# Performance work log

Measured on AMD Instinct MI355X. Metric: run time of the kernel, lower is better.

The kernel has to match this reference:

```python
import jax, jax.numpy as jnp
import numpy as np

EMBED = 1024
HEADS = 16
HDIM = EMBED // HEADS
QLEN = 512
KLEN = 1024
BATCH = 8


def setup_inputs() -> dict:
    key = jax.random.key(0)
    ks = jax.random.split(key, 20)
    s = 0.02
    return {
        "query": jax.random.normal(ks[0], (QLEN, BATCH, EMBED), jnp.float32),
        "key": jax.random.normal(ks[1], (KLEN, BATCH, EMBED), jnp.float32),
        "value": jax.random.normal(ks[2], (KLEN, BATCH, EMBED), jnp.float32),
        "pos_embedding": jax.random.normal(ks[3], (KLEN, 1, EMBED), jnp.float32),
        "U": jax.random.normal(ks[4], (HEADS, HDIM), jnp.float32) * s,
        "V": jax.random.normal(ks[5], (HEADS, HDIM), jnp.float32) * s,
        "mask": jax.random.randint(ks[6], (QLEN, KLEN, 1), 0, 2) == 1,
        "padding_mask": jax.random.randint(ks[7], (BATCH, QLEN), 0, 2).astype(jnp.float32),
        "Wq": jax.random.normal(ks[8], (EMBED, EMBED), jnp.float32) * s,
        "bq": jnp.zeros((EMBED,), jnp.float32),
        "Wk": jax.random.normal(ks[9], (EMBED, EMBED), jnp.float32) * s,
        "bk": jnp.zeros((EMBED,), jnp.float32),
        "Wv": jax.random.normal(ks[10], (EMBED, EMBED), jnp.float32) * s,
        "bv": jnp.zeros((EMBED,), jnp.float32),
        "Wpos": jax.random.normal(ks[11], (EMBED, EMBED), jnp.float32) * s,
        "Wo": jax.random.normal(ks[12], (EMBED, EMBED), jnp.float32) * s,
        "bo": jnp.zeros((EMBED,), jnp.float32),
    }


def _rel_shift(x):
    # x: (q, k, b, h) -> Transformer-XL relative shift (pad/reshape trick)
    q, k, b, h = x.shape
    zero_pad = jnp.zeros((q, 1, b, h), x.dtype)
    x_padded = jnp.concatenate([zero_pad, x], axis=1)  # (q, k+1, b, h)
    x_padded = x_padded.reshape(k + 1, q, b, h)
    return x_padded[1:].reshape(q, k, b, h)


def _padding_mask(pad, q_len, k_len):
    # pad: (b, q) in {0,1}; returns bool (b, q, k) where True = masked
    pm = jnp.einsum('bq,bk->bqk', pad, pad)  # (b, q, q)
    if k_len > q_len:
        mem = jnp.ones((pad.shape[0], q_len, k_len - q_len), pad.dtype)
        pm = jnp.concatenate([mem, pm], axis=2)
    return pm == 0


def reference(query, key, value, pos_embedding, U, V, mask, padding_mask,
              Wq, bq, Wk, bk, Wv, bv, Wpos, Wo, bo):
    q_len, b, e = query.shape
    k_len = key.shape[0]
    d = jnp.asarray(np.sqrt(e), query.dtype)

    q = (query @ Wq + bq).reshape(q_len, b, HEADS, HDIM)
    k = (key @ Wk + bk).reshape(k_len, b, HEADS, HDIM)
    v = (value @ Wv + bv).reshape(k_len, b, HEADS, HDIM)
    R = (pos_embedding @ Wpos).reshape(-1, HEADS, HDIM)  # (k_len, h, d)

    content = jnp.einsum('qbhd,kbhd->qkbh', q + U, k)
    position = _rel_shift(jnp.einsum('qbhd,khd->qkbh', q + V, R))
    score = (content + position) / d  # (q, k, b, h)

    NEG = jnp.asarray(-1e20, score.dtype)
    score = jnp.where(mask[:, :, :, None], NEG, score)  # mask (q,k,1)->(q,k,1,1)
    pmask = _padding_mask(padding_mask, q_len, k_len)  # (b,q,k)
    pmask = jnp.transpose(pmask, (1, 2, 0))[:, :, :, None]  # (q,k,b,1)
    score = jnp.where(pmask, NEG, score)

    attn = jax.nn.softmax(score, axis=1)
    alpha = jnp.einsum('qkbh,kbhd->qbhd', attn, v).reshape(q_len, b, e)
    return alpha @ Wo + bo
```

## Files before the change

### kernel.cpp

```cpp
#include <hip/hip_runtime.h>

#define QLEN 512
#define KLEN 1024
#define BATCH 8
#define HEADS 16
#define HDIM 64
#define EMBED 1024

typedef __attribute__((ext_vector_type(4))) float f32x4;
typedef __attribute__((ext_vector_type(8))) short short8;
typedef unsigned short ushort_t;
typedef unsigned char uchar_t;
typedef unsigned int uint_t;

#define MFMA16(a, b, c) __builtin_amdgcn_mfma_f32_16x16x32_bf16((a), (b), (c), 0, 0, 0)

__device__ __forceinline__ float b2f(ushort_t u) {
    union { uint_t i; float f; } c; c.i = ((uint_t)u) << 16; return c.f;
}
__device__ __forceinline__ ushort_t f2b(float x) {
    union { float f; uint_t i; } c; c.f = x;
    return (ushort_t)((c.i + 0x8000u) >> 16);
}
__device__ __forceinline__ uint_t pk2(float lo, float hi) {
    return (uint_t)f2b(lo) | ((uint_t)f2b(hi) << 16);
}
__device__ __forceinline__ float ldf(const void* p, int idx, int f32m) {
    if (f32m) return ((const float*)p)[idx];
    return b2f(((const ushort_t*)p)[idx]);
}

typedef const __attribute__((address_space(1))) void async_src_t;
typedef __attribute__((address_space(3))) void async_dst_t;

__global__ __launch_bounds__(256) void detect_kernel(const void* mask, const void* pad, int* flags) {
    __shared__ int cnt[4];
    int tid = threadIdx.x;
    if (tid < 4) cnt[tid] = 0;
    __syncthreads();
    const uchar_t* mb = (const uchar_t*)mask;
    const uchar_t* pb = (const uchar_t*)pad;
    int lnz1 = 0, l3f1 = 0, l3f3 = 0, lpnz = 0;
    for (int off = tid; off < 4096; off += 256) {
        uchar_t v = mb[off];
        int m4 = off & 3;
        if (m4 != 0 && v != 0) lnz1++;
        if (m4 == 1 && v == 0x3F) l3f1++;
        if (m4 == 3 && v == 0x3F) l3f3++;
        uchar_t p = pb[off];
        if (m4 == 0 && p != 0) lpnz++;
    }
    atomicAdd(&cnt[0], lnz1); atomicAdd(&cnt[1], l3f1);
    atomicAdd(&cnt[2], l3f3); atomicAdd(&cnt[3], lpnz);
    __syncthreads();
    if (tid == 0) {
        flags[0] = (cnt[3] == 0) ? 1 : 0;
        int mm;
        if (cnt[0] == 0) mm = 0;
        else if (cnt[1] > 16) mm = 2;
        else if (cnt[2] > 16) mm = 3;
        else mm = 1;
        flags[1] = mm;
    }
}

__device__ __forceinline__ void conv_body(const void* __restrict__ src, ushort_t* __restrict__ dst,
                                          int i, int n8, int f32m) {
    if (i >= n8) return;
    if (f32m) {
        const float4* s = (const float4*)src + (size_t)i * 2;
        float4 a = s[0], b = s[1];
        uint4 o;
        o.x = pk2(a.x, a.y); o.y = pk2(a.z, a.w);
        o.z = pk2(b.x, b.y); o.w = pk2(b.z, b.w);
        ((uint4*)dst)[i] = o;
    } else {
        ((uint4*)dst)[i] = ((const uint4*)src)[i];
    }
}

__global__ __launch_bounds__(256) void prep_kernel(
    const void* q_in, ushort_t* qbf, const void* k_in, ushort_t* kbf,
    const void* v_in, ushort_t* vbf,
    const void* W0, const void* W1, const void* W2, const void* W3, const void* W4,
    ushort_t* T0, ushort_t* T1, ushort_t* T2, ushort_t* T3, ushort_t* T4,
    const int* flags) {
    __shared__ float tl[32][33];
    const int bid = blockIdx.x;
    const int tid = threadIdx.x;
    const int f32m = flags[0];
    if (bid < 2048) {
        conv_body(q_in, qbf, bid * 256 + tid, 524288, f32m);
    } else if (bid < 6144) {
        conv_body(k_in, kbf, (bid - 2048) * 256 + tid, 1048576, f32m);
    } else if (bid < 10240) {
        conv_body(v_in, vbf, (bid - 6144) * 256 + tid, 1048576, f32m);
    } else {
        int l = bid - 10240;
        int z = l >> 10, r = l & 1023;
        int bx = r & 31, by = r >> 5;
        const void* W; ushort_t* T;
        switch (z) {
            case 0: W = W0; T = T0; break;
            case 1: W = W1; T = T1; break;
            case 2: W = W2; T = T2; break;
            case 3: W = W3; T = T3; break;
            default: W = W4; T = T4; break;
        }
        int tx = tid & 31, ty = tid >> 5;
        int x = bx * 32 + tx;
        #pragma unroll
        for (int j = 0; j < 4; ++j) {
            int row = by * 32 + ty + j * 8;
            tl[ty + j * 8][tx] = ldf(W, row * 1024 + x, f32m);
        }
        __syncthreads();
        #pragma unroll
        for (int j = 0; j < 4; ++j) {
            int n = bx * 32 + ty + j * 8;
            T[n * 1024 + by * 32 + tx] = f2b(tl[tx][ty + j * 8]);
        }
    }
}

template<int EPI>
__device__ __forceinline__ void gemm_body(
    int mt, int nt, const void* Av, const ushort_t* BT,
    const void* bias, const void* Up, const void* Vp,
    void* out0, void* out1, const int* flags, int a_mode,
    ushort_t* As, ushort_t* Bs) {
    const int f32m = flags[0];
    const int a_f32 = a_mode ? f32m : 0;
    const int tid = threadIdx.x;
    const int wid = tid >> 6, lane = tid & 63;
    const int wr = (wid >> 1) * 64, wc = (wid & 1) * 64;
    const int m0 = mt * 128, n0 = nt * 128;
    const int ch0 = wid * 2;
    const int lrow = lane >> 2, lcol = (lane & 3) * 8;

    f32x4 acc[4][4];
    #pragma unroll
    for (int m = 0; m < 4; ++m)
        #pragma unroll
        for (int n = 0; n < 4; ++n)
            acc[m][n] = (f32x4){0.f, 0.f, 0.f, 0.f};

    for (int k0 = 0; k0 < 1024; k0 += 32) {
        if (a_f32) {
            const float* Af = (const float*)Av + (size_t)(m0 + (tid >> 1)) * 1024 + k0 + (tid & 1) * 16;
            ushort_t* dst = &As[(tid >> 1) * 32 + (tid & 1) * 16];
            #pragma unroll
            for (int e = 0; e < 16; ++e) dst[e] = f2b(Af[e]);
        } else {
            #pragma unroll
            for (int t = 0; t < 2; ++t) {
                int ch = ch0 + t;
                const ushort_t* ga = (const ushort_t*)Av + (size_t)(m0 + ch * 16 + lrow) * 1024 + k0 + lcol;
                __builtin_amdgcn_global_load_lds((async_src_t*)ga, (async_dst_t*)&As[ch * 512], 16, 0, 0);
            }
        }
        #pragma unroll
        for (int t = 0; t < 2; ++t) {
            int ch = ch0 + t;
            const ushort_t* gb = BT + (size_t)(n0 + ch * 16 + lrow) * 1024 + k0 + lcol;
            __builtin_amdgcn_global_load_lds((async_src_t*)gb, (async_dst_t*)&Bs[ch * 512], 16, 0, 0);
        }
        __syncthreads();

        short8 af[4], bf[4];
        #pragma unroll
        for (int m = 0; m < 4; ++m)
            af[m] = *(const short8*)&As[(wr + m * 16 + (lane & 15)) * 32 + (lane >> 4) * 8];
        #pragma unroll
        for (int n = 0; n < 4; ++n)
            bf[n] = *(const short8*)&Bs[(wc + n * 16 + (lane & 15)) * 32 + (lane >> 4) * 8];
        #pragma unroll
        for (int m = 0; m < 4; ++m)
            #pragma unroll
            for (int n = 0; n < 4; ++n)
                acc[m][n] = MFMA16(af[m], bf[n], acc[m][n]);
        __syncthreads();
    }

    #pragma unroll
    for (int n = 0; n < 4; ++n) {
        int gn = n0 + wc + n * 16 + (lane & 15);
        float bv_ = (EPI == 2) ? 0.f : ldf(bias, gn, f32m);
        float uu = 0.f, vv = 0.f;
        if (EPI == 0) { uu = ldf(Up, gn, f32m); vv = ldf(Vp, gn, f32m); }
        #pragma unroll
        for (int m = 0; m < 4; ++m) {
            #pragma unroll
            for (int j = 0; j < 4; ++j) {
                int gm = m0 + wr + m * 16 + (lane >> 4) * 4 + j;
                float c = acc[m][n][j] + bv_;
                if (EPI == 0) {
                    int q = gm >> 3, b = gm & 7;
                    int h = gn >> 6, d = gn & 63;
                    int bhk = b * 16 + h;
                    size_t addr = ((size_t)bhk * 32 + (q >> 4)) * 1024 + (size_t)(d >> 5) * 512
                                  + ((q & 15) * 4 + ((d >> 3) & 3)) * 8 + (d & 7);
                    ((ushort_t*)out0)[addr] = f2b((c + uu) * 0.03125f);
                    ((ushort_t*)out1)[addr] = f2b((c + vv) * 0.03125f);
                } else if (EPI == 1) {
                    int kk = gm >> 3, b = gm & 7;
                    int h = gn >> 6, d = gn & 63;
                    ((ushort_t*)out0)[((b * 16 + h) * 1024 + kk) * 64 + d] = f2b(c);
                } else if (EPI == 2) {
                    int h = gn >> 6, d = gn & 63;
                    int jr = gm;
                    size_t addr = (((((size_t)h * 8 + (jr >> 7)) * 8 + ((jr >> 4) & 7)) * 2 + (d >> 5)) * 64
                                   + ((jr & 15) * 4 + ((d >> 3) & 3))) * 8 + (d & 7);
                    ((ushort_t*)out0)[addr] = f2b(c);
                } else if (EPI == 4) {
                    int kk = gm >> 3, b = gm & 7;
                    int h = gn >> 6, d = gn & 63;
                    size_t addr = ((((((size_t)(b * 16 + h)) * 8 + (kk >> 7)) * 8 + ((kk >> 4) & 7)) * 2 + (d >> 5)) * 64
                                   + ((kk & 15) * 4 + ((d >> 3) & 3))) * 8 + (d & 7);
                    ((ushort_t*)out0)[addr] = f2b(c);
                } else {
                    if (f32m) ((float*)out0)[gm * 1024 + gn] = c;
                    else ((ushort_t*)out0)[gm * 1024 + gn] = f2b(c);
                }
            }
        }
    }
}

template<int EPI>
__global__ __launch_bounds__(256) void gemm_kernel(
    const void* Av, const ushort_t* BT, int M,
    const void* bias, const void* Up, const void* Vp,
    void* out0, void* out1, const int* flags, int a_mode) {
    __shared__ ushort_t As[4096];
    __shared__ ushort_t Bs[4096];
    gemm_body<EPI>(blockIdx.x, blockIdx.y, Av, BT, bias, Up, Vp, out0, out1, flags, a_mode, As, Bs);
}

__global__ __launch_bounds__(256) void proj1_kernel(
    const ushort_t* qbf, const ushort_t* WqT, const void* bq, const void* Up, const void* Vp,
    ushort_t* qUw, ushort_t* qVw,
    const ushort_t* kbf, const ushort_t* WkT, const void* bk, ushort_t* khw,
    const void* pos_raw, const ushort_t* WposT, ushort_t* Rlw,
    const int* flags) {
    __shared__ ushort_t As[4096];
    __shared__ ushort_t Bs[4096];
    const int bid = blockIdx.x;
    if (bid < 256) {
        gemm_body<0>(bid & 31, bid >> 5, qbf, WqT, bq, Up, Vp, qUw, qVw, flags, 0, As, Bs);
    } else if (bid < 768) {
        int l = bid - 256;
        gemm_body<4>(l & 63, l >> 6, kbf, WkT, bk, nullptr, nullptr, khw, nullptr, flags, 0, As, Bs);
    } else {
        int l = bid - 768;
        gemm_body<2>(l & 7, l >> 3, pos_raw, WposT, nullptr, nullptr, nullptr, Rlw, nullptr, flags, 1, As, Bs);
    }
}

__global__ __launch_bounds__(256) void preattn_kernel(
    const ushort_t* __restrict__ vh, ushort_t* __restrict__ vT,
    const void* __restrict__ mask, const void* __restrict__ pad,
    uint_t* __restrict__ bits, const int* flags) {
    __shared__ ushort_t t[64][68];
    const int bid = blockIdx.x;
    const int tid = threadIdx.x;
    if (bid < 2048) {
        int bh = bid >> 4;
        int k0 = (bid & 15) * 64;
        int r = tid >> 2, c0 = (tid & 3) * 16;
        const short8* src = (const short8*)&vh[((size_t)bh * 1024 + k0 + r) * 64 + c0];
        *(short8*)&t[r][c0] = src[0];
        *(short8*)&t[r][c0 + 8] = src[1];
        __syncthreads();
        ushort_t tmp[16];
        #pragma unroll
        for (int j = 0; j < 16; ++j) tmp[j] = t[c0 + j][r];
        int dm = r >> 4, cc = r & 15;
        #pragma unroll
        for (int tt = 0; tt < 2; ++tt) {
            int og = ((k0 + c0) >> 3) + tt;
            int kc = og >> 4, ch = (og >> 2) & 3, g = og & 3;
            size_t addr = ((((((size_t)bh * 8 + kc) * 4 + ch) * 4 + dm) * 64) + cc * 4 + g) * 8;
            *(short8*)&vT[addr] = *(short8*)&tmp[tt * 8];
        }
    } else {
        int tid2 = (bid - 2048) * 256 + tid;
        int w = tid2 & 31, q = (tid2 >> 5) & 511, b = tid2 >> 14;
        int mm = flags[1], f32m = flags[0];
        float padq = ldf(pad, b * 512 + q, f32m);
        uint_t word = 0;
        for (int j = 0; j < 32; ++j) {
            int k = w * 32 + j;
            size_t mi = (size_t)q * 1024 + k;
            int dead;
            if (mm == 1) dead = (((const uchar_t*)mask)[mi] != 0);
            else if (mm == 2) dead = (((const ushort_t*)mask)[mi] != 0);
            else dead = (((const uint_t*)mask)[mi] != 0);
            if (k >= 512) {
                float padk = ldf(pad, b * 512 + k - 512, f32m);
                if (padq == 0.f || padk == 0.f) dead = 1;
            }
            word |= ((uint_t)dead) << j;
        }
        bits[((b * 8 + (w >> 2)) * 512 + q) * 4 + (w & 3)] = word;
    }
}

#define SP_STR 1032
#define PB_STR 136
__global__ __launch_bounds__(512, 4) void attn_kernel(
    const ushort_t* __restrict__ qU, const ushort_t* __restrict__ qV,
    const ushort_t* __restrict__ khn, const ushort_t* __restrict__ vtn,
    const ushort_t* __restrict__ Rln, const uint_t* __restrict__ mbits,
    ushort_t* __restrict__ alpha) {

    __shared__ __align__(16) uchar_t uni[35104];
    ushort_t* sPos = (ushort_t*)uni;
    ushort_t* sPb  = (ushort_t*)uni;
    float*    sO   = (float*)uni;
    __shared__ float sred[2][8][16];
    __shared__ float ssinv[16];

    const int tid = threadIdx.x;
    const int wid = tid >> 6, lane = tid & 63;
    const int g = lane >> 4, c = lane & 15;
    const int qt = blockIdx.x;
    const int q0 = qt * 16;
    const int bh = blockIdx.y;
    const int b = bh >> 4, h = bh & 15;
    const int kbase = wid * 128;
    const int lch = (c * 4 + g) * 8;

    {
        size_t qvb = ((size_t)bh * 32 + qt) * 1024;
        short8 bva0 = *(const short8*)&qV[qvb + lch];
        short8 bva1 = *(const short8*)&qV[qvb + 512 + lch];
        int qtb = (qt == 31) ? 31 : qt + 1;
        int cb = (qt == 31) ? 15 : c;
        size_t qvb2 = ((size_t)bh * 32 + qtb) * 1024;
        short8 bvb0 = *(const short8*)&qV[qvb2 + (cb * 4 + g) * 8];
        short8 bvb1 = *(const short8*)&qV[qvb2 + 512 + (cb * 4 + g) * 8];
        #pragma unroll
        for (int m = 0; m < 8; ++m) {
            size_t rb = ((((size_t)h * 8 + wid) * 8 + m) * 2) * 512;
            short8 ra0 = *(const short8*)&Rln[rb + lch];
            short8 ra1 = *(const short8*)&Rln[rb + 512 + lch];
            f32x4 p0 = (f32x4){0.f, 0.f, 0.f, 0.f};
            p0 = MFMA16(ra0, bva0, p0);
            p0 = MFMA16(ra1, bva1, p0);
            f32x4 p1 = (f32x4){0.f, 0.f, 0.f, 0.f};
            p1 = MFMA16(ra0, bvb0, p1);
            p1 = MFMA16(ra1, bvb1, p1);
            uint2 w;
            w.x = pk2(p0[0], p0[1]);
            w.y = pk2(p0[2], p0[3]);
            *(uint2*)&sPos[c * SP_STR + kbase + m * 16 + g * 4] = w;
            if (c == 0) {
                uint2 x;
                x.x = pk2(p1[0], p1[1]);
                x.y = pk2(p1[2], p1[3]);
                *(uint2*)&sPos[16 * SP_STR + kbase + m * 16 + g * 4] = x;
            }
        }
    }

    f32x4 acc[8];
    {
        size_t qub = ((size_t)bh * 32 + qt) * 1024;
        short8 bu0 = *(const short8*)&qU[qub + lch];
        short8 bu1 = *(const short8*)&qU[qub + 512 + lch];
        #pragma unroll
        for (int m = 0; m < 8; ++m) {
            size_t kb = ((((size_t)bh * 8 + wid) * 8 + m) * 2) * 512;
            short8 ka0 = *(const short8*)&khn[kb + lch];
            short8 ka1 = *(const short8*)&khn[kb + 512 + lch];
            f32x4 t = (f32x4){0.f, 0.f, 0.f, 0.f};
            t = MFMA16(ka0, bu0, t);
            t = MFMA16(ka1, bu1, t);
            acc[m] = t;
        }
    }
    __syncthreads();

    const int q = q0 + c;
    uint4 mw = *(const uint4*)(mbits + ((size_t)(b * 8 + wid) * 512 + q) * 4);
    uint_t mwa[4] = {mw.x, mw.y, mw.z, mw.w};

    const int mbase = kbase - q0;
    float mx = -3.0e38f;
    #pragma unroll
    for (int m = 0; m < 8; ++m) {
        const int mb = mbase + m * 16;
        uint_t word = mwa[m >> 1];
        if (mb + 15 <= 512) {
            int a0 = c * SP_STR + mb + g * 4 - c + 511;
            #pragma unroll
            for (int jj = 0; jj < 4; ++jj) {
                float s = acc[m][jj] + b2f(sPos[a0 + jj]);
                if ((word >> ((m & 1) * 16 + g * 4 + jj)) & 1u) s = -1e20f;
                acc[m][jj] = s;
                mx = fmaxf(mx, s);
            }
        } else if (mb - 15 >= 514) {
            int a0 = (c + 1) * SP_STR + mb + g * 4 - c - 514;
            #pragma unroll
            for (int jj = 0; jj < 4; ++jj) {
                float s = acc[m][jj] + b2f(sPos[a0 + jj]);
                if ((word >> ((m & 1) * 16 + g * 4 + jj)) & 1u) s = -1e20f;
                acc[m][jj] = s;
                mx = fmaxf(mx, s);
            }
        } else {
            #pragma unroll
            for (int jj = 0; jj < 4; ++jj) {
                int delta = mb + g * 4 + jj - c;
                int wrap = (delta > 512) ? 1 : 0;
                int j = wrap ? (delta - 514) : (delta + 511);
                float pos = b2f(sPos[(c + wrap) * SP_STR + j]);
                if (delta == 513) pos = 0.f;
                float s = acc[m][jj] + pos;
                if ((word >> ((m & 1) * 16 + g * 4 + jj)) & 1u) s = -1e20f;
                acc[m][jj] = s;
                mx = fmaxf(mx, s);
            }
        }
    }
    mx = fmaxf(mx, __shfl_xor(mx, 16, 64));
    mx = fmaxf(mx, __shfl_xor(mx, 32, 64));
    if (lane < 16) sred[0][wid][c] = mx;
    __syncthreads();
    {
        float a0 = fmaxf(fmaxf(sred[0][0][c], sred[0][1][c]), fmaxf(sred[0][2][c], sred[0][3][c]));
        float a1 = fmaxf(fmaxf(sred[0][4][c], sred[0][5][c]), fmaxf(sred[0][6][c], sred[0][7][c]));
        mx = fmaxf(a0, a1);
    }

    float ls = 0.f;
    #pragma unroll
    for (int m = 0; m < 8; ++m) {
        float p0 = __expf(acc[m][0] - mx);
        float p1 = __expf(acc[m][1] - mx);
        float p2 = __expf(acc[m][2] - mx);
        float p3 = __expf(acc[m][3] - mx);
        ls += (p0 + p1) + (p2 + p3);
        uint2 w;
        w.x = pk2(p0, p1);
        w.y = pk2(p2, p3);
        *(uint2*)&sPb[(wid * 16 + c) * PB_STR + m * 16 + g * 4] = w;
    }
    ls += __shfl_xor(ls, 16, 64);
    ls += __shfl_xor(ls, 32, 64);
    if (lane < 16) sred[1][wid][c] = ls;

    short8 va[4][4];
    #pragma unroll
    for (int ch = 0; ch < 4; ++ch)
        #pragma unroll
        for (int dm = 0; dm < 4; ++dm)
            va[ch][dm] = *(const short8*)&vtn[((((((size_t)bh * 8 + wid) * 4 + ch) * 4 + dm) * 64) * 8) + lch];
    __syncthreads();
    float ls2;
    {
        float a0 = (sred[1][0][c] + sred[1][1][c]) + (sred[1][2][c] + sred[1][3][c]);
        float a1 = (sred[1][4][c] + sred[1][5][c]) + (sred[1][6][c] + sred[1][7][c]);
        ls2 = a0 + a1;
    }
    if (wid == 0 && lane < 16) ssinv[c] = 1.0f / ls2;

    f32x4 oacc[4];
    #pragma unroll
    for (int dm = 0; dm < 4; ++dm) oacc[dm] = (f32x4){0.f, 0.f, 0.f, 0.f};
    short8 pbv[4];
    #pragma unroll
    for (int ch = 0; ch < 4; ++ch)
        pbv[ch] = *(const short8*)&sPb[(wid * 16 + c) * PB_STR + ch * 32 + g * 8];
    #pragma unroll
    for (int ch = 0; ch < 4; ++ch)
        #pragma unroll
        for (int dm = 0; dm < 4; ++dm)
            oacc[dm] = MFMA16(va[ch][dm], pbv[ch], oacc[dm]);

    __syncthreads();
    #pragma unroll
    for (int dm = 0; dm < 4; ++dm)
        #pragma unroll
        for (int jj = 0; jj < 4; ++jj)
            sO[wid * 1088 + (dm * 16 + g * 4 + jj) * 17 + c] = oacc[dm][jj];
    __syncthreads();
    for (int e = tid; e < 1024; e += 512) {
        int d = e & 63, qq = e >> 6;
        float v = ((sO[d * 17 + qq] + sO[1088 + d * 17 + qq]) +
                   (sO[2176 + d * 17 + qq] + sO[3264 + d * 17 + qq])) +
                  ((sO[4352 + d * 17 + qq] + sO[5440 + d * 17 + qq]) +
                   (sO[6528 + d * 17 + qq] + sO[7616 + d * 17 + qq]));
        v *= ssinv[qq];
        alpha[((size_t)(q0 + qq) * 8 + b) * 1024 + h * 64 + d] = f2b(v);
    }
}

extern "C" void kernel_launch(void* const* d_in, const int* in_sizes, int n_in,
                              void* d_out, int out_size, void* d_ws, size_t ws_size,
                              hipStream_t stream) {
    char* ws = (char*)d_ws;
    int* flags = (int*)ws;
    ushort_t* WqT   = (ushort_t*)(ws + 1024);
    ushort_t* WkT   = WqT + 1048576;
    ushort_t* WvT   = WkT + 1048576;
    ushort_t* WposT = WvT + 1048576;
    ushort_t* WoT   = WposT + 1048576;
    ushort_t* qUw   = WoT + 1048576;
    ushort_t* qVw   = qUw + 4194304;
    ushort_t* khw   = qVw + 4194304;
    ushort_t* Rlw   = khw + 8388608;
    ushort_t* R1    = Rlw + 1048576;
    ushort_t* R2    = R1 + 4194304;
    ushort_t* R3    = R2 + 8388608;
    ushort_t* qbf = R1;
    ushort_t* alw = R1;
    ushort_t* kbf = R2;
    ushort_t* vhw = R2;
    ushort_t* vbf = R3;
    ushort_t* vTw = R3;
    uint_t* mbits = (uint_t*)WqT;

    detect_kernel<<<1, 256, 0, stream>>>(d_in[6], d_in[7], flags);
    prep_kernel<<<15360, 256, 0, stream>>>(
        d_in[0], qbf, d_in[1], kbf, d_in[2], vbf,
        d_in[8], d_in[10], d_in[12], d_in[14], d_in[15],
        WqT, WkT, WvT, WposT, WoT, flags);
    proj1_kernel<<<832, 256, 0, stream>>>(
        qbf, WqT, d_in[9], d_in[4], d_in[5], qUw, qVw,
        kbf, WkT, d_in[11], khw,
        d_in[3], WposT, Rlw, flags);
    gemm_kernel<1><<<dim3(64, 8), 256, 0, stream>>>(vbf, WvT, 8192, d_in[13], nullptr, nullptr, vhw, nullptr, flags, 0);
    preattn_kernel<<<2560, 256, 0, stream>>>(vhw, vTw, d_in[6], d_in[7], mbits, flags);
    attn_kernel<<<dim3(32, 128), 512, 0, stream>>>(qUw, qVw, khw, vTw, Rlw, mbits, alw);
    gemm_kernel<3><<<dim3(32, 8), 256, 0, stream>>>(alw, WoT, 4096, d_in[16], nullptr, nullptr, d_out, nullptr, flags, 0);
}
```

Baseline: 316.6 us.

## Fuse V projection with transpose and mask build; use 64-row tiles for small GEMMs

The V projection GEMM now writes directly into the transposed tiled layout that attention consumes, which removes the separate transpose pass and its extra global round trip. It is merged with the mask-bit construction into one launch. A 64x128-tile GEMM variant is added for the Q projection and the output projection, doubling their block counts so more compute units are busy on these M=4096 GEMMs. The cost is scattered epilogue stores for V and a lower per-block reuse in the smaller tiles.

```diff
diff --git a/kernel.cpp b/kernel.cpp
--- a/kernel.cpp
+++ b/kernel.cpp
@@ -126,8 +126,7 @@
 template<int EPI>
 __device__ __forceinline__ void gemm_body(
     int mt, int nt, const void* Av, const ushort_t* BT,
-    const void* bias, const void* Up, const void* Vp,
-    void* out0, void* out1, const int* flags, int a_mode,
+    const void* bias, void* out0, const int* flags, int a_mode,
     ushort_t* As, ushort_t* Bs) {
     const int f32m = flags[0];
     const int a_f32 = a_mode ? f32m : 0;
@@ -186,27 +185,13 @@
     for (int n = 0; n < 4; ++n) {
         int gn = n0 + wc + n * 16 + (lane & 15);
         float bv_ = (EPI == 2) ? 0.f : ldf(bias, gn, f32m);
-        float uu = 0.f, vv = 0.f;
-        if (EPI == 0) { uu = ldf(Up, gn, f32m); vv = ldf(Vp, gn, f32m); }
         #pragma unroll
         for (int m = 0; m < 4; ++m) {
             #pragma unroll
             for (int j = 0; j < 4; ++j) {
                 int gm = m0 + wr + m * 16 + (lane >> 4) * 4 + j;
                 float c = acc[m][n][j] + bv_;
-                if (EPI == 0) {
-                    int q = gm >> 3, b = gm & 7;
-                    int h = gn >> 6, d = gn & 63;
-                    int bhk = b * 16 + h;
-                    size_t addr = ((size_t)bhk * 32 + (q >> 4)) * 1024 + (size_t)(d >> 5) * 512
-                                  + ((q & 15) * 4 + ((d >> 3) & 3)) * 8 + (d & 7);
-                    ((ushort_t*)out0)[addr] = f2b((c + uu) * 0.03125f);
-                    ((ushort_t*)out1)[addr] = f2b((c + vv) * 0.03125f);
-                } else if (EPI == 1) {
-                    int kk = gm >> 3, b = gm & 7;
-                    int h = gn >> 6, d = gn & 63;
-                    ((ushort_t*)out0)[((b * 16 + h) * 1024 + kk) * 64 + d] = f2b(c);
-                } else if (EPI == 2) {
+                if (EPI == 2) {
                     int h = gn >> 6, d = gn & 63;
                     int jr = gm;
                     size_t addr = (((((size_t)h * 8 + (jr >> 7)) * 8 + ((jr >> 4) & 7)) * 2 + (d >> 5)) * 64
@@ -219,22 +204,95 @@
                                    + ((kk & 15) * 4 + ((d >> 3) & 3))) * 8 + (d & 7);
                     ((ushort_t*)out0)[addr] = f2b(c);
                 } else {
+                    int kk = gm >> 3, b = gm & 7;
+                    int h = gn >> 6, d = gn & 63;
+                    int bh = b * 16 + h;
+                    int kc = kk >> 7, ch2 = (kk >> 5) & 3, gg = (kk >> 3) & 3, e = kk & 7;
+                    int dm = d >> 4, cc = d & 15;
+                    size_t addr = ((((((size_t)bh * 8 + kc) * 4 + ch2) * 4 + dm) * 64) + cc * 4 + gg) * 8 + e;
+                    ((ushort_t*)out0)[addr] = f2b(c);
+                }
+            }
+        }
+    }
+}
+
+template<int EPI>
+__device__ __forceinline__ void gemm_body64(
+    int mt, int nt, const void* Av, const ushort_t* BT,
+    const void* bias, const void* Up, const void* Vp,
+    void* out0, void* out1, const int* flags,
+    ushort_t* As, ushort_t* Bs) {
+    const int f32m = flags[0];
+    const int tid = threadIdx.x;
+    const int wid = tid >> 6, lane = tid & 63;
+    const int wr = (wid >> 1) * 32, wc = (wid & 1) * 64;
+    const int m0 = mt * 64, n0 = nt * 128;
+    const int ch0 = wid * 2;
+    const int lrow = lane >> 2, lcol = (lane & 3) * 8;
+
+    f32x4 acc[2][4];
+    #pragma unroll
+    for (int m = 0; m < 2; ++m)
+        #pragma unroll
+        for (int n = 0; n < 4; ++n)
+            acc[m][n] = (f32x4){0.f, 0.f, 0.f, 0.f};
+
+    for (int k0 = 0; k0 < 1024; k0 += 32) {
+        {
+            const ushort_t* ga = (const ushort_t*)Av + (size_t)(m0 + wid * 16 + lrow) * 1024 + k0 + lcol;
+            __builtin_amdgcn_global_load_lds((async_src_t*)ga, (async_dst_t*)&As[wid * 512], 16, 0, 0);
+        }
+        #pragma unroll
+        for (int t = 0; t < 2; ++t) {
+            int ch = ch0 + t;
+            const ushort_t* gb = BT + (size_t)(n0 + ch * 16 + lrow) * 1024 + k0 + lcol;
+            __builtin_amdgcn_global_load_lds((async_src_t*)gb, (async_dst_t*)&Bs[ch * 512], 16, 0, 0);
+        }
+        __syncthreads();
+
+        short8 af[2], bf[4];
+        #pragma unroll
+        for (int m = 0; m < 2; ++m)
+            af[m] = *(const short8*)&As[(wr + m * 16 + (lane & 15)) * 32 + (lane >> 4) * 8];
+        #pragma unroll
+        for (int n = 0; n < 4; ++n)
+            bf[n] = *(const short8*)&Bs[(wc + n * 16 + (lane & 15)) * 32 + (lane >> 4) * 8];
+        #pragma unroll
+        for (int m = 0; m < 2; ++m)
+            #pragma unroll
+            for (int n = 0; n < 4; ++n)
+                acc[m][n] = MFMA16(af[m], bf[n], acc[m][n]);
+        __syncthreads();
+    }
+
+    #pragma unroll
+    for (int n = 0; n < 4; ++n) {
+        int gn = n0 + wc + n * 16 + (lane & 15);
+        float bv_ = ldf(bias, gn, f32m);
+        float uu = 0.f, vv = 0.f;
+        if (EPI == 0) { uu = ldf(Up, gn, f32m); vv = ldf(Vp, gn, f32m); }
+        #pragma unroll
+        for (int m = 0; m < 2; ++m) {
+            #pragma unroll
+            for (int j = 0; j < 4; ++j) {
+                int gm = m0 + wr + m * 16 + (lane >> 4) * 4 + j;
+                float c = acc[m][n][j] + bv_;
+                if (EPI == 0) {
+                    int q = gm >> 3, b = gm & 7;
+                    int h = gn >> 6, d = gn & 63;
+                    int bhk = b * 16 + h;
+                    size_t addr = ((size_t)bhk * 32 + (q >> 4)) * 1024 + (size_t)(d >> 5) * 512
+                                  + ((q & 15) * 4 + ((d >> 3) & 3)) * 8 + (d & 7);
+                    ((ushort_t*)out0)[addr] = f2b((c + uu) * 0.03125f);
+                    ((ushort_t*)out1)[addr] = f2b((c + vv) * 0.03125f);
+                } else {
                     if (f32m) ((float*)out0)[gm * 1024 + gn] = c;
                     else ((ushort_t*)out0)[gm * 1024 + gn] = f2b(c);
                 }
             }
         }
     }
-}
-
-template<int EPI>
-__global__ __launch_bounds__(256) void gemm_kernel(
-    const void* Av, const ushort_t* BT, int M,
-    const void* bias, const void* Up, const void* Vp,
-    void* out0, void* out1, const int* flags, int a_mode) {
-    __shared__ ushort_t As[4096];
-    __shared__ ushort_t Bs[4096];
-    gemm_body<EPI>(blockIdx.x, blockIdx.y, Av, BT, bias, Up, Vp, out0, out1, flags, a_mode, As, Bs);
 }
 
 __global__ __launch_bounds__(256) void proj1_kernel(
@@ -246,45 +304,29 @@
     __shared__ ushort_t As[4096];
     __shared__ ushort_t Bs[4096];
     const int bid = blockIdx.x;
-    if (bid < 256) {
-        gemm_body<0>(bid & 31, bid >> 5, qbf, WqT, bq, Up, Vp, qUw, qVw, flags, 0, As, Bs);
-    } else if (bid < 768) {
-        int l = bid - 256;
-        gemm_body<4>(l & 63, l >> 6, kbf, WkT, bk, nullptr, nullptr, khw, nullptr, flags, 0, As, Bs);
+    if (bid < 512) {
+        gemm_body64<0>(bid & 63, bid >> 6, qbf, WqT, bq, Up, Vp, qUw, qVw, flags, As, Bs);
+    } else if (bid < 1024) {
+        int l = bid - 512;
+        gemm_body<4>(l & 63, l >> 6, kbf, WkT, bk, khw, flags, 0, As, Bs);
     } else {
-        int l = bid - 768;
-        gemm_body<2>(l & 7, l >> 3, pos_raw, WposT, nullptr, nullptr, nullptr, Rlw, nullptr, flags, 1, As, Bs);
-    }
-}
-
-__global__ __launch_bounds__(256) void preattn_kernel(
-    const ushort_t* __restrict__ vh, ushort_t* __restrict__ vT,
+        int l = bid - 1024;
+        gemm_body<2>(l & 7, l >> 3, pos_raw, WposT, nullptr, Rlw, flags, 1, As, Bs);
+    }
+}
+
+__global__ __launch_bounds__(256) void vmask_kernel(
+    const ushort_t* vbf, const ushort_t* WvT, const void* bv, ushort_t* vT,
     const void* __restrict__ mask, const void* __restrict__ pad,
     uint_t* __restrict__ bits, const int* flags) {
-    __shared__ ushort_t t[64][68];
+    __shared__ ushort_t As[4096];
+    __shared__ ushort_t Bs[4096];
     const int bid = blockIdx.x;
     const int tid = threadIdx.x;
-    if (bid < 2048) {
-        int bh = bid >> 4;
-        int k0 = (bid & 15) * 64;
-        int r = tid >> 2, c0 = (tid & 3) * 16;
-        const short8* src = (const short8*)&vh[((size_t)bh * 1024 + k0 + r) * 64 + c0];
-        *(short8*)&t[r][c0] = src[0];
-        *(short8*)&t[r][c0 + 8] = src[1];
-        __syncthreads();
-        ushort_t tmp[16];
-        #pragma unroll
-        for (int j = 0; j < 16; ++j) tmp[j] = t[c0 + j][r];
-        int dm = r >> 4, cc = r & 15;
-        #pragma unroll
-        for (int tt = 0; tt < 2; ++tt) {
-            int og = ((k0 + c0) >> 3) + tt;
-            int kc = og >> 4, ch = (og >> 2) & 3, g = og & 3;
-            size_t addr = ((((((size_t)bh * 8 + kc) * 4 + ch) * 4 + dm) * 64) + cc * 4 + g) * 8;
-            *(short8*)&vT[addr] = *(short8*)&tmp[tt * 8];
-        }
+    if (bid < 512) {
+        gemm_body<5>(bid & 63, bid >> 6, vbf, WvT, bv, vT, flags, 0, As, Bs);
     } else {
-        int tid2 = (bid - 2048) * 256 + tid;
+        int tid2 = (bid - 512) * 256 + tid;
         int w = tid2 & 31, q = (tid2 >> 5) & 511, b = tid2 >> 14;
         int mm = flags[1], f32m = flags[0];
         float padq = ldf(pad, b * 512 + q, f32m);
@@ -304,6 +346,13 @@
         }
         bits[((b * 8 + (w >> 2)) * 512 + q) * 4 + (w & 3)] = word;
     }
+}
+
+__global__ __launch_bounds__(256) void outgemm_kernel(
+    const ushort_t* Av, const ushort_t* BT, const void* bias, void* out0, const int* flags) {
+    __shared__ ushort_t As[4096];
+    __shared__ ushort_t Bs[4096];
+    gemm_body64<3>(blockIdx.x, blockIdx.y, Av, BT, bias, nullptr, nullptr, out0, nullptr, flags, As, Bs);
 }
 
 #define SP_STR 1032
@@ -518,9 +567,8 @@
     ushort_t* qbf = R1;
     ushort_t* alw = R1;
     ushort_t* kbf = R2;
-    ushort_t* vhw = R2;
+    ushort_t* vTw = R2;
     ushort_t* vbf = R3;
-    ushort_t* vTw = R3;
     uint_t* mbits = (uint_t*)WqT;
 
     detect_kernel<<<1, 256, 0, stream>>>(d_in[6], d_in[7], flags);
@@ -528,12 +576,12 @@
         d_in[0], qbf, d_in[1], kbf, d_in[2], vbf,
         d_in[8], d_in[10], d_in[12], d_in[14], d_in[15],
         WqT, WkT, WvT, WposT, WoT, flags);
-    proj1_kernel<<<832, 256, 0, stream>>>(
+    proj1_kernel<<<1088, 256, 0, stream>>>(
         qbf, WqT, d_in[9], d_in[4], d_in[5], qUw, qVw,
         kbf, WkT, d_in[11], khw,
         d_in[3], WposT, Rlw, flags);
-    gemm_kernel<1><<<dim3(64, 8), 256, 0, stream>>>(vbf, WvT, 8192, d_in[13], nullptr, nullptr, vhw, nullptr, flags, 0);
-    preattn_kernel<<<2560, 256, 0, stream>>>(vhw, vTw, d_in[6], d_in[7], mbits, flags);
+    vmask_kernel<<<1024, 256, 0, stream>>>(
+        vbf, WvT, d_in[13], vTw, d_in[6], d_in[7], mbits, flags);
     attn_kernel<<<dim3(32, 128), 512, 0, stream>>>(qUw, qVw, khw, vTw, Rlw, mbits, alw);
-    gemm_kernel<3><<<dim3(32, 8), 256, 0, stream>>>(alw, WoT, 4096, d_in[16], nullptr, nullptr, d_out, nullptr, flags, 0);
-}
+    outgemm_kernel<<<dim3(64, 8), 256, 0, stream>>>(alw, WoT, d_in[16], d_out, flags);
+}
```

Result: slower. 328.0 us (+3.6%).
